# Optimization experiments

Hardware: AMD Instinct MI355X
Metric: run time of the kernel (lower is better)

The kernel has to match this reference:

```python
import jax, jax.numpy as jnp
import numpy as np

B, S, D, H = 4, 2048, 1024, 16
DK = D // H
NEG = -1000000000.0


def setup_inputs() -> dict:
    key = jax.random.key(0)
    ks = jax.random.split(key, 12)
    scale = 1.0 / np.sqrt(D)
    inp = {
        "query": jax.random.normal(ks[0], (B, S, D), jnp.float32),
        "key": jax.random.normal(ks[1], (B, S, D), jnp.float32),
        "value": jax.random.normal(ks[2], (B, S, D), jnp.float32),
        "mask": jax.random.randint(ks[3], (B, S, S), 0, 2, jnp.int32),
        "Wq": jax.random.normal(ks[4], (D, D), jnp.float32) * scale,
        "bq": jnp.zeros((D,), jnp.float32),
        "Wk": jax.random.normal(ks[5], (D, D), jnp.float32) * scale,
        "bk": jnp.zeros((D,), jnp.float32),
        "Wv": jax.random.normal(ks[6], (D, D), jnp.float32) * scale,
        "bv": jnp.zeros((D,), jnp.float32),
        "Wo": jax.random.normal(ks[7], (D, D), jnp.float32) * scale,
        "bo": jnp.zeros((D,), jnp.float32),
    }
    return inp


def _split_heads(x):
    # (B, S, D) -> (B, H, S, DK)
    return x.reshape(B, -1, H, DK).transpose(0, 2, 1, 3)


def reference(query, key, value, mask, Wq, bq, Wk, bk, Wv, bv, Wo, bo):
    q = _split_heads(query @ Wq.T + bq)
    k = _split_heads(key @ Wk.T + bk)
    v = _split_heads(value @ Wv.T + bv)
    scores = jnp.einsum('bhqd,bhkd->bhqk', q, k) / jnp.sqrt(jnp.float32(DK))
    scores = jnp.where(mask[:, None, :, :] == 0, NEG, scores)
    p_attn = jax.nn.softmax(scores, axis=-1)
    x = jnp.einsum('bhqk,bhkd->bhqd', p_attn, v)
    x = x.transpose(0, 2, 1, 3).reshape(B, -1, D)
    return x @ Wo.T + bo
```

## Files before the change

kernel.cpp:

```cpp
#include <hip/hip_runtime.h>

#define BDIM 4
#define SDIM 2048
#define DDIM 1024
#define HDIM 16
#define DKDIM 64
#define MDIM (BDIM*SDIM)

typedef __attribute__((ext_vector_type(8))) short bf16x8_t;
typedef __attribute__((ext_vector_type(4))) float f32x4_t;

__device__ __forceinline__ unsigned short f2bf(float f) {
    union { float f; unsigned u; } v; v.f = f;
    unsigned r = v.u + 0x7FFFu + ((v.u >> 16) & 1u);
    return (unsigned short)(r >> 16);
}

__device__ __forceinline__ unsigned pkbf(float a, float b) {
#if defined(__has_builtin) && __has_builtin(__builtin_amdgcn_cvt_pk_bf16_f32)
    auto v = __builtin_amdgcn_cvt_pk_bf16_f32(a, b);
    union { decltype(v) x; unsigned u; } cv; cv.x = v; return cv.u;
#else
    return (unsigned)f2bf(a) | ((unsigned)f2bf(b) << 16);
#endif
}

#if defined(__has_builtin) && __has_builtin(__builtin_amdgcn_exp2f)
#define EXP2F(x) __builtin_amdgcn_exp2f(x)
#else
#define EXP2F(x) __expf((x) * 0.69314718f)
#endif

__device__ __forceinline__ void gl_lds16(const void* g, void* l) {
    __builtin_amdgcn_global_load_lds(
        (const __attribute__((address_space(1))) unsigned int*)g,
        (__attribute__((address_space(3))) unsigned int*)l, 16, 0, 0);
}

__global__ void cvt3(const float* __restrict__ a, const float* __restrict__ b, const float* __restrict__ c,
                     unsigned short* __restrict__ oa, unsigned short* __restrict__ ob, unsigned short* __restrict__ oc,
                     int n4) {
    int i = blockIdx.x * blockDim.x + threadIdx.x;
    const float* s = blockIdx.y == 0 ? a : (blockIdx.y == 1 ? b : c);
    unsigned short* d = blockIdx.y == 0 ? oa : (blockIdx.y == 1 ? ob : oc);
    if (i < n4) {
        float4 v = ((const float4*)s)[i];
        ushort4 o;
        o.x = f2bf(v.x); o.y = f2bf(v.y); o.z = f2bf(v.z); o.w = f2bf(v.w);
        ((ushort4*)d)[i] = o;
    }
}

__global__ void cvt4(const float* __restrict__ a, const float* __restrict__ b,
                     const float* __restrict__ c, const float* __restrict__ e,
                     unsigned short* __restrict__ oa, unsigned short* __restrict__ ob,
                     unsigned short* __restrict__ oc, unsigned short* __restrict__ oe,
                     int n4) {
    int i = blockIdx.x * blockDim.x + threadIdx.x;
    const float* s = blockIdx.y == 0 ? a : (blockIdx.y == 1 ? b : (blockIdx.y == 2 ? c : e));
    unsigned short* d = blockIdx.y == 0 ? oa : (blockIdx.y == 1 ? ob : (blockIdx.y == 2 ? oc : oe));
    if (i < n4) {
        float4 v = ((const float4*)s)[i];
        ushort4 o;
        o.x = f2bf(v.x); o.y = f2bf(v.y); o.z = f2bf(v.z); o.w = f2bf(v.w);
        ((ushort4*)d)[i] = o;
    }
}

__global__ void pack_mask(const int* __restrict__ m, unsigned long long* __restrict__ bits) {
    int g = blockIdx.x * 256 + threadIdx.x;
    unsigned long long bal = __ballot(m[g] != 0);
    if ((threadIdx.x & 63) == 0) bits[g >> 6] = bal;
}

template<int OMODE>
__global__ __launch_bounds__(256) void gemm_nt(
    const unsigned short* __restrict__ A,
    const unsigned short* __restrict__ B,
    const float* __restrict__ bias,
    unsigned short* __restrict__ Cb,
    float* __restrict__ Cf,
    int M, int N, int K)
{
    __shared__ unsigned short As[128 * 32];
    __shared__ unsigned short Bs[128 * 32];
    const int tid = threadIdx.x;
    const int w = tid >> 6, lane = tid & 63;
    const int wr = w >> 1, wc = w & 1;
    const int quad = lane >> 4, l16 = lane & 15;
    const int bn = blockIdx.x, bm = blockIdx.y;

    const int rl = lane >> 2, cl = (lane & 3) * 8;
    const int c0 = w * 2;
    const unsigned short* gA = A + (size_t)(bm * 128 + c0 * 16 + rl) * K + cl;
    const unsigned short* gB = B + (size_t)(bn * 128 + c0 * 16 + rl) * K + cl;
    unsigned short* lA = As + c0 * 512 + lane * 8;
    unsigned short* lB = Bs + c0 * 512 + lane * 8;

    f32x4_t acc[4][4] = {};

    for (int k0 = 0; k0 < K; k0 += 32) {
        gl_lds16(gA, lA);
        gl_lds16(gA + (size_t)16 * K, lA + 16 * 32);
        gl_lds16(gB, lB);
        gl_lds16(gB + (size_t)16 * K, lB + 16 * 32);
        gA += 32; gB += 32;
        __syncthreads();
        bf16x8_t af[4], bfr[4];
#pragma unroll
        for (int mi = 0; mi < 4; ++mi)
            af[mi] = *(const bf16x8_t*)(As + (wr * 64 + mi * 16 + l16) * 32 + quad * 8);
#pragma unroll
        for (int ni = 0; ni < 4; ++ni)
            bfr[ni] = *(const bf16x8_t*)(Bs + (wc * 64 + ni * 16 + l16) * 32 + quad * 8);
#pragma unroll
        for (int mi = 0; mi < 4; ++mi)
#pragma unroll
            for (int ni = 0; ni < 4; ++ni)
                acc[mi][ni] = __builtin_amdgcn_mfma_f32_16x16x32_bf16(af[mi], bfr[ni], acc[mi][ni], 0, 0, 0);
        __syncthreads();
    }

#pragma unroll
    for (int mi = 0; mi < 4; ++mi) {
#pragma unroll
        for (int ni = 0; ni < 4; ++ni) {
            const int n = bn * 128 + wc * 64 + ni * 16 + l16;
            const int m0 = bm * 128 + wr * 64 + mi * 16 + quad * 4;
            const float bv = bias[n];
            if (OMODE == 1) {
                ushort4 pk;
                pk.x = f2bf(acc[mi][ni][0] + bv);
                pk.y = f2bf(acc[mi][ni][1] + bv);
                pk.z = f2bf(acc[mi][ni][2] + bv);
                pk.w = f2bf(acc[mi][ni][3] + bv);
                *(ushort4*)(Cb + (size_t)n * M + m0) = pk;
            } else {
#pragma unroll
                for (int r = 0; r < 4; ++r) {
                    const float v = acc[mi][ni][r] + bv;
                    if (OMODE == 0) Cb[(size_t)(m0 + r) * N + n] = f2bf(v);
                    else            Cf[(size_t)(m0 + r) * N + n] = v;
                }
            }
        }
    }
}

__global__ __launch_bounds__(256) void attn_kernel(
    const unsigned short* __restrict__ Qp,
    const unsigned short* __restrict__ Kp,
    const unsigned short* __restrict__ Vt,
    const unsigned long long* __restrict__ mbits,
    unsigned short* __restrict__ Xa)
{
    __shared__ unsigned short Ks[2 * 64 * 32];
    __shared__ unsigned short Vs[2 * 64 * 32];
    __shared__ __align__(16) float Pf[4][2][16][36];

    const int tid = threadIdx.x, w = tid >> 6, lane = tid & 63;
    const int quad = lane >> 4, l16 = lane & 15;
    const int bx = blockIdx.x;
    const int h = bx & 15, qt = (bx >> 4) & 31, b = bx >> 9;
    const int q0 = qt * 64;
    const int rl = lane >> 2, cl = (lane & 3) * 8;

#pragma unroll
    for (int i = 0; i < 2; ++i) {
        const int cc = w * 2 + i;
        const int row = b * SDIM + q0 + (cc & 3) * 16 + rl;
        const int col = h * 64 + (cc >> 2) * 32 + cl;
        gl_lds16(Qp + (size_t)row * DDIM + col, Ks + cc * 512 + lane * 8);
    }
    __syncthreads();
    bf16x8_t aq[2];
    aq[0] = *(const bf16x8_t*)(Ks + 0 * 2048 + (w * 16 + l16) * 32 + quad * 8);
    aq[1] = *(const bf16x8_t*)(Ks + 1 * 2048 + (w * 16 + l16) * 32 + quad * 8);

    const unsigned long long* mb_base =
        mbits + (size_t)(b * SDIM + q0 + w * 16 + quad * 4) * 32;

    float l_part[4] = {0.f, 0.f, 0.f, 0.f};
    f32x4_t o[4] = {};

    for (int kt = 0; kt < SDIM / 64; ++kt) {
        __syncthreads();
#pragma unroll
        for (int i = 0; i < 2; ++i) {
            const int cc = w * 2 + i;
            const int rowk = b * SDIM + kt * 64 + (cc & 3) * 16 + rl;
            const int colk = h * 64 + (cc >> 2) * 32 + cl;
            gl_lds16(Kp + (size_t)rowk * DDIM + colk, Ks + cc * 512 + lane * 8);
            const int rowv = h * 64 + (cc & 3) * 16 + rl;
            const int colv = b * SDIM + kt * 64 + (cc >> 2) * 32 + cl;
            gl_lds16(Vt + (size_t)rowv * MDIM + colv, Vs + cc * 512 + lane * 8);
        }
        __syncthreads();

        unsigned long long mb[4];
#pragma unroll
        for (int r = 0; r < 4; ++r) mb[r] = mb_base[r * 32 + kt];

        f32x4_t sf[4] = {};
#pragma unroll
        for (int kk = 0; kk < 2; ++kk) {
#pragma unroll
            for (int ni = 0; ni < 4; ++ni) {
                const bf16x8_t bk = *(const bf16x8_t*)(Ks + kk * 2048 + (ni * 16 + l16) * 32 + quad * 8);
                sf[ni] = __builtin_amdgcn_mfma_f32_16x16x32_bf16(aq[kk], bk, sf[ni], 0, 0, 0);
            }
        }

#pragma unroll
        for (int ni = 0; ni < 4; ++ni) {
#pragma unroll
            for (int r = 0; r < 4; ++r) {
                float t = sf[ni][r] * 0.18033688f;
                t = ((mb[r] >> (ni * 16 + l16)) & 1ull) ? t : -1.0e9f;
                const float p = EXP2F(t);
                l_part[r] += p;
                Pf[w][ni >> 1][quad * 4 + r][(ni & 1) * 16 + l16] = p;
            }
        }

#pragma unroll
        for (int kk = 0; kk < 2; ++kk) {
            const float* pr = &Pf[w][kk][l16][quad * 8];
            const float4 p0 = *(const float4*)pr;
            const float4 p1 = *(const float4*)(pr + 4);
            union { unsigned u[4]; bf16x8_t v; } fu;
            fu.u[0] = pkbf(p0.x, p0.y);
            fu.u[1] = pkbf(p0.z, p0.w);
            fu.u[2] = pkbf(p1.x, p1.y);
            fu.u[3] = pkbf(p1.z, p1.w);
#pragma unroll
            for (int ni = 0; ni < 4; ++ni) {
                const bf16x8_t bv = *(const bf16x8_t*)(Vs + kk * 2048 + (ni * 16 + l16) * 32 + quad * 8);
                o[ni] = __builtin_amdgcn_mfma_f32_16x16x32_bf16(fu.v, bv, o[ni], 0, 0, 0);
            }
        }
    }

#pragma unroll
    for (int off = 1; off < 16; off <<= 1)
#pragma unroll
        for (int r = 0; r < 4; ++r)
            l_part[r] += __shfl_xor(l_part[r], off, 64);

    float rcp[4];
#pragma unroll
    for (int r = 0; r < 4; ++r) rcp[r] = 1.0f / l_part[r];
#pragma unroll
    for (int ni = 0; ni < 4; ++ni)
#pragma unroll
        for (int r = 0; r < 4; ++r) {
            const int qg = q0 + w * 16 + quad * 4 + r;
            const int cg = h * 64 + ni * 16 + l16;
            Xa[((size_t)b * SDIM + qg) * DDIM + cg] = f2bf(o[ni][r] * rcp[r]);
        }
}

extern "C" void kernel_launch(void* const* d_in, const int* in_sizes, int n_in,
                              void* d_out, int out_size, void* d_ws, size_t ws_size,
                              hipStream_t stream)
{
    const float* query = (const float*)d_in[0];
    const float* key   = (const float*)d_in[1];
    const float* value = (const float*)d_in[2];
    const int*   mask  = (const int*)d_in[3];
    const float* Wq = (const float*)d_in[4];  const float* bq = (const float*)d_in[5];
    const float* Wk = (const float*)d_in[6];  const float* bk = (const float*)d_in[7];
    const float* Wv = (const float*)d_in[8];  const float* bv = (const float*)d_in[9];
    const float* Wo = (const float*)d_in[10]; const float* bo = (const float*)d_in[11];

    const size_t MD = (size_t)MDIM * DDIM;
    const size_t DD = (size_t)DDIM * DDIM;

    unsigned short* qb  = (unsigned short*)d_ws;
    unsigned short* kb  = qb + MD;
    unsigned short* vb  = kb + MD;
    unsigned short* wqb = vb + MD;
    unsigned short* wkb = wqb + DD;
    unsigned short* wvb = wkb + DD;
    unsigned short* wob = wvb + DD;
    unsigned short* Qp  = wob + DD;
    unsigned short* Kp  = Qp + MD;
    unsigned short* Vt  = Kp + MD;
    unsigned short* Xa  = Vt + MD;
    unsigned long long* mbits = (unsigned long long*)qb;

    {
        const int n4m = (int)(MD / 4), n4d = (int)(DD / 4);
        dim3 g3((n4m + 255) / 256, 3), g4((n4d + 255) / 256, 4);
        cvt3<<<g3, 256, 0, stream>>>(query, key, value, qb, kb, vb, n4m);
        cvt4<<<g4, 256, 0, stream>>>(Wq, Wk, Wv, Wo, wqb, wkb, wvb, wob, n4d);
    }

    dim3 gg(DDIM / 128, MDIM / 128);
    gemm_nt<0><<<gg, 256, 0, stream>>>(qb, wqb, bq, Qp, nullptr, MDIM, DDIM, DDIM);
    gemm_nt<0><<<gg, 256, 0, stream>>>(kb, wkb, bk, Kp, nullptr, MDIM, DDIM, DDIM);
    gemm_nt<1><<<gg, 256, 0, stream>>>(vb, wvb, bv, Vt, nullptr, MDIM, DDIM, DDIM);

    pack_mask<<<(BDIM * SDIM * SDIM) / 256, 256, 0, stream>>>(mask, mbits);

    attn_kernel<<<BDIM * HDIM * (SDIM / 64), 256, 0, stream>>>(Qp, Kp, Vt, mbits, Xa);

    gemm_nt<2><<<gg, 256, 0, stream>>>(Xa, wob, bo, nullptr, (float*)d_out, MDIM, DDIM, DDIM);
}
```

Before: 496.8 us.

## Double attention query tile per block and compute row sums via MFMA

The attention kernel now handles 128 query rows per block, with 32 per wave, so each loaded K/V tile feeds twice as many MFMAs. This halves global K/V traffic per query. The softmax scale is folded into the Q projection epilogue, and masked entries become -inf. Row sums now come from an extra MFMA against a ones vector instead of scalar accumulation plus shuffles. In exchange, the grid has half as many blocks and each block uses more registers and LDS, which could lower occupancy. The change also relies on every row having at least one unmasked key to avoid a zero denominator.

```diff
diff --git a/kernel.cpp b/kernel.cpp
--- a/kernel.cpp
+++ b/kernel.cpp
@@ -30,6 +30,8 @@
 #else
 #define EXP2F(x) __expf((x) * 0.69314718f)
 #endif
+
+#define QSCALE 0.18033688011112042f
 
 __device__ __forceinline__ void gl_lds16(const void* g, void* l) {
     __builtin_amdgcn_global_load_lds(
@@ -80,7 +82,7 @@
     const float* __restrict__ bias,
     unsigned short* __restrict__ Cb,
     float* __restrict__ Cf,
-    int M, int N, int K)
+    int M, int N, int K, float scale)
 {
     __shared__ unsigned short As[128 * 32];
     __shared__ unsigned short Bs[128 * 32];
@@ -130,15 +132,15 @@
             const float bv = bias[n];
             if (OMODE == 1) {
                 ushort4 pk;
-                pk.x = f2bf(acc[mi][ni][0] + bv);
-                pk.y = f2bf(acc[mi][ni][1] + bv);
-                pk.z = f2bf(acc[mi][ni][2] + bv);
-                pk.w = f2bf(acc[mi][ni][3] + bv);
+                pk.x = f2bf((acc[mi][ni][0] + bv) * scale);
+                pk.y = f2bf((acc[mi][ni][1] + bv) * scale);
+                pk.z = f2bf((acc[mi][ni][2] + bv) * scale);
+                pk.w = f2bf((acc[mi][ni][3] + bv) * scale);
                 *(ushort4*)(Cb + (size_t)n * M + m0) = pk;
             } else {
 #pragma unroll
                 for (int r = 0; r < 4; ++r) {
-                    const float v = acc[mi][ni][r] + bv;
+                    const float v = (acc[mi][ni][r] + bv) * scale;
                     if (OMODE == 0) Cb[(size_t)(m0 + r) * N + n] = f2bf(v);
                     else            Cf[(size_t)(m0 + r) * N + n] = v;
                 }
@@ -156,32 +158,38 @@
 {
     __shared__ unsigned short Ks[2 * 64 * 32];
     __shared__ unsigned short Vs[2 * 64 * 32];
-    __shared__ __align__(16) float Pf[4][2][16][36];
+    __shared__ __align__(16) float Pf[4][2][2][16][36];
 
     const int tid = threadIdx.x, w = tid >> 6, lane = tid & 63;
     const int quad = lane >> 4, l16 = lane & 15;
     const int bx = blockIdx.x;
-    const int h = bx & 15, qt = (bx >> 4) & 31, b = bx >> 9;
-    const int q0 = qt * 64;
+    const int h = bx & 15, qt = (bx >> 4) & 15, b = bx >> 8;
+    const int q0 = qt * 128;
     const int rl = lane >> 2, cl = (lane & 3) * 8;
 
 #pragma unroll
-    for (int i = 0; i < 2; ++i) {
-        const int cc = w * 2 + i;
-        const int row = b * SDIM + q0 + (cc & 3) * 16 + rl;
-        const int col = h * 64 + (cc >> 2) * 32 + cl;
-        gl_lds16(Qp + (size_t)row * DDIM + col, Ks + cc * 512 + lane * 8);
+    for (int i = 0; i < 4; ++i) {
+        const int cc = w * 4 + i;
+        const int row = b * SDIM + q0 + (cc & 7) * 16 + rl;
+        const int col = h * 64 + (cc >> 3) * 32 + cl;
+        unsigned short* dst = (cc < 8 ? Ks + cc * 512 : Vs + (cc - 8) * 512) + lane * 8;
+        gl_lds16(Qp + (size_t)row * DDIM + col, dst);
     }
     __syncthreads();
-    bf16x8_t aq[2];
-    aq[0] = *(const bf16x8_t*)(Ks + 0 * 2048 + (w * 16 + l16) * 32 + quad * 8);
-    aq[1] = *(const bf16x8_t*)(Ks + 1 * 2048 + (w * 16 + l16) * 32 + quad * 8);
-
-    const unsigned long long* mb_base =
-        mbits + (size_t)(b * SDIM + q0 + w * 16 + quad * 4) * 32;
-
-    float l_part[4] = {0.f, 0.f, 0.f, 0.f};
-    f32x4_t o[4] = {};
+    bf16x8_t aq[2][2];
+#pragma unroll
+    for (int g = 0; g < 2; ++g) {
+        aq[g][0] = *(const bf16x8_t*)(Ks + (w * 2 + g) * 512 + l16 * 32 + quad * 8);
+        aq[g][1] = *(const bf16x8_t*)(Vs + (w * 2 + g) * 512 + l16 * 32 + quad * 8);
+    }
+
+    const unsigned long long* mp =
+        mbits + (size_t)(b * SDIM + q0 + w * 32 + quad * 4) * 32;
+
+    f32x4_t o[2][4] = {};
+    f32x4_t o4[2] = {};
+    union { unsigned u[4]; bf16x8_t v; } ones;
+    ones.u[0] = ones.u[1] = ones.u[2] = ones.u[3] = 0x3F803F80u;
 
     for (int kt = 0; kt < SDIM / 64; ++kt) {
         __syncthreads();
@@ -197,67 +205,80 @@
         }
         __syncthreads();
 
-        unsigned long long mb[4];
-#pragma unroll
-        for (int r = 0; r < 4; ++r) mb[r] = mb_base[r * 32 + kt];
-
-        f32x4_t sf[4] = {};
+        unsigned long long mb[2][4];
+#pragma unroll
+        for (int g = 0; g < 2; ++g)
+#pragma unroll
+            for (int r = 0; r < 4; ++r) mb[g][r] = mp[g * 512 + r * 32 + kt];
+
+        f32x4_t sf[2][4] = {};
 #pragma unroll
         for (int kk = 0; kk < 2; ++kk) {
 #pragma unroll
             for (int ni = 0; ni < 4; ++ni) {
                 const bf16x8_t bk = *(const bf16x8_t*)(Ks + kk * 2048 + (ni * 16 + l16) * 32 + quad * 8);
-                sf[ni] = __builtin_amdgcn_mfma_f32_16x16x32_bf16(aq[kk], bk, sf[ni], 0, 0, 0);
-            }
-        }
-
-#pragma unroll
-        for (int ni = 0; ni < 4; ++ni) {
+                sf[0][ni] = __builtin_amdgcn_mfma_f32_16x16x32_bf16(aq[0][kk], bk, sf[0][ni], 0, 0, 0);
+                sf[1][ni] = __builtin_amdgcn_mfma_f32_16x16x32_bf16(aq[1][kk], bk, sf[1][ni], 0, 0, 0);
+            }
+        }
+
+#pragma unroll
+        for (int g = 0; g < 2; ++g) {
 #pragma unroll
             for (int r = 0; r < 4; ++r) {
-                float t = sf[ni][r] * 0.18033688f;
-                t = ((mb[r] >> (ni * 16 + l16)) & 1ull) ? t : -1.0e9f;
-                const float p = EXP2F(t);
-                l_part[r] += p;
-                Pf[w][ni >> 1][quad * 4 + r][(ni & 1) * 16 + l16] = p;
+                const unsigned long long sh = mb[g][r] >> l16;
+                const unsigned mlo = (unsigned)sh;
+                const unsigned mhi = (unsigned)(sh >> 32);
+                const int row = quad * 4 + r;
+                const float t0 = (mlo & 1u)         ? sf[g][0][r] : -INFINITY;
+                const float t1 = ((mlo >> 16) & 1u) ? sf[g][1][r] : -INFINITY;
+                const float t2 = (mhi & 1u)         ? sf[g][2][r] : -INFINITY;
+                const float t3 = ((mhi >> 16) & 1u) ? sf[g][3][r] : -INFINITY;
+                Pf[w][g][0][row][l16]      = EXP2F(t0);
+                Pf[w][g][0][row][16 + l16] = EXP2F(t1);
+                Pf[w][g][1][row][l16]      = EXP2F(t2);
+                Pf[w][g][1][row][16 + l16] = EXP2F(t3);
             }
         }
 
 #pragma unroll
         for (int kk = 0; kk < 2; ++kk) {
-            const float* pr = &Pf[w][kk][l16][quad * 8];
-            const float4 p0 = *(const float4*)pr;
-            const float4 p1 = *(const float4*)(pr + 4);
-            union { unsigned u[4]; bf16x8_t v; } fu;
-            fu.u[0] = pkbf(p0.x, p0.y);
-            fu.u[1] = pkbf(p0.z, p0.w);
-            fu.u[2] = pkbf(p1.x, p1.y);
-            fu.u[3] = pkbf(p1.z, p1.w);
-#pragma unroll
-            for (int ni = 0; ni < 4; ++ni) {
-                const bf16x8_t bv = *(const bf16x8_t*)(Vs + kk * 2048 + (ni * 16 + l16) * 32 + quad * 8);
-                o[ni] = __builtin_amdgcn_mfma_f32_16x16x32_bf16(fu.v, bv, o[ni], 0, 0, 0);
-            }
-        }
-    }
-
-#pragma unroll
-    for (int off = 1; off < 16; off <<= 1)
-#pragma unroll
-        for (int r = 0; r < 4; ++r)
-            l_part[r] += __shfl_xor(l_part[r], off, 64);
-
-    float rcp[4];
-#pragma unroll
-    for (int r = 0; r < 4; ++r) rcp[r] = 1.0f / l_part[r];
-#pragma unroll
-    for (int ni = 0; ni < 4; ++ni)
-#pragma unroll
-        for (int r = 0; r < 4; ++r) {
-            const int qg = q0 + w * 16 + quad * 4 + r;
-            const int cg = h * 64 + ni * 16 + l16;
-            Xa[((size_t)b * SDIM + qg) * DDIM + cg] = f2bf(o[ni][r] * rcp[r]);
-        }
+            bf16x8_t bvf[4];
+#pragma unroll
+            for (int ni = 0; ni < 4; ++ni)
+                bvf[ni] = *(const bf16x8_t*)(Vs + kk * 2048 + (ni * 16 + l16) * 32 + quad * 8);
+#pragma unroll
+            for (int g = 0; g < 2; ++g) {
+                const float* pr = &Pf[w][g][kk][l16][quad * 8];
+                const float4 pa = *(const float4*)pr;
+                const float4 pb = *(const float4*)(pr + 4);
+                union { unsigned u[4]; bf16x8_t v; } fu;
+                fu.u[0] = pkbf(pa.x, pa.y);
+                fu.u[1] = pkbf(pa.z, pa.w);
+                fu.u[2] = pkbf(pb.x, pb.y);
+                fu.u[3] = pkbf(pb.z, pb.w);
+#pragma unroll
+                for (int ni = 0; ni < 4; ++ni)
+                    o[g][ni] = __builtin_amdgcn_mfma_f32_16x16x32_bf16(fu.v, bvf[ni], o[g][ni], 0, 0, 0);
+                o4[g] = __builtin_amdgcn_mfma_f32_16x16x32_bf16(fu.v, ones.v, o4[g], 0, 0, 0);
+            }
+        }
+    }
+
+#pragma unroll
+    for (int g = 0; g < 2; ++g) {
+        float rcp[4];
+#pragma unroll
+        for (int r = 0; r < 4; ++r) rcp[r] = 1.0f / o4[g][r];
+#pragma unroll
+        for (int ni = 0; ni < 4; ++ni)
+#pragma unroll
+            for (int r = 0; r < 4; ++r) {
+                const int qg = q0 + w * 32 + g * 16 + quad * 4 + r;
+                const int cg = h * 64 + ni * 16 + l16;
+                Xa[((size_t)b * SDIM + qg) * DDIM + cg] = f2bf(o[g][ni][r] * rcp[r]);
+            }
+    }
 }
 
 extern "C" void kernel_launch(void* const* d_in, const int* in_sizes, int n_in,
@@ -297,13 +318,13 @@
     }
 
     dim3 gg(DDIM / 128, MDIM / 128);
-    gemm_nt<0><<<gg, 256, 0, stream>>>(qb, wqb, bq, Qp, nullptr, MDIM, DDIM, DDIM);
-    gemm_nt<0><<<gg, 256, 0, stream>>>(kb, wkb, bk, Kp, nullptr, MDIM, DDIM, DDIM);
-    gemm_nt<1><<<gg, 256, 0, stream>>>(vb, wvb, bv, Vt, nullptr, MDIM, DDIM, DDIM);
+    gemm_nt<0><<<gg, 256, 0, stream>>>(qb, wqb, bq, Qp, nullptr, MDIM, DDIM, DDIM, QSCALE);
+    gemm_nt<0><<<gg, 256, 0, stream>>>(kb, wkb, bk, Kp, nullptr, MDIM, DDIM, DDIM, 1.0f);
+    gemm_nt<1><<<gg, 256, 0, stream>>>(vb, wvb, bv, Vt, nullptr, MDIM, DDIM, DDIM, 1.0f);
 
     pack_mask<<<(BDIM * SDIM * SDIM) / 256, 256, 0, stream>>>(mask, mbits);
 
-    attn_kernel<<<BDIM * HDIM * (SDIM / 64), 256, 0, stream>>>(Qp, Kp, Vt, mbits, Xa);
-
-    gemm_nt<2><<<gg, 256, 0, stream>>>(Xa, wob, bo, nullptr, (float*)d_out, MDIM, DDIM, DDIM);
-}
+    attn_kernel<<<BDIM * HDIM * (SDIM / 128), 256, 0, stream>>>(Qp, Kp, Vt, mbits, Xa);
+
+    gemm_nt<2><<<gg, 256, 0, stream>>>(Xa, wob, bo, nullptr, (float*)d_out, MDIM, DDIM, DDIM, 1.0f);
+}
```

Result: no change. 499.7 us (+0.6%).
